# Optimization experiments

Hardware: AMD Instinct MI355X
Metric: run time of the kernel (lower is better)

The kernel has to match this reference:

```python
import jax, jax.numpy as jnp
import numpy as np

T, B, S = 8, 4, 2048
LAT, SYM, NC = 1024, 256, 512


def setup_inputs() -> dict:
    key = jax.random.key(0)
    ks = jax.random.split(key, 16)
    inp = {
        "token_state": jax.random.normal(ks[0], (B, S, LAT), jnp.float32),
        "bus_symbols": jax.random.normal(ks[1], (T, B, S, SYM), jnp.float32),
        "bus_indices": jax.random.randint(ks[2], (T, B, S), 0, NC),
        "bus_outputs": jax.random.normal(ks[3], (T, B, S, LAT), jnp.float32),
        "bus_mask": jnp.zeros((T,), jnp.bool_),
        # parameters (stored as (in, out) matrices)
        "Wq": jax.random.normal(ks[4], (SYM, 1), jnp.float32) / np.sqrt(SYM),
        "bq": jnp.zeros((1,), jnp.float32),
        "Wread": jax.random.normal(ks[5], (2 * LAT, LAT), jnp.float32) / np.sqrt(2 * LAT),
        "bread": jnp.zeros((LAT,), jnp.float32),
        "Wsym": jax.random.normal(ks[6], (LAT, SYM), jnp.float32) / np.sqrt(LAT),
        "bsym": jnp.zeros((SYM,), jnp.float32),
        "Wc1": jax.random.normal(ks[7], (LAT + SYM, LAT), jnp.float32) / np.sqrt(LAT + SYM),
        "bc1": jnp.zeros((LAT,), jnp.float32),
        "Wc2": jax.random.normal(ks[8], (LAT, LAT), jnp.float32) / np.sqrt(LAT),
        "bc2": jnp.zeros((LAT,), jnp.float32),
        "codebook": jax.random.normal(ks[9], (NC, SYM), jnp.float32),
    }
    return inp


def reference(token_state, bus_symbols, bus_indices, bus_outputs, bus_mask,
              Wq, bq, Wread, bread, Wsym, bsym, Wc1, bc1, Wc2, bc2, codebook):
    Tm, Bb, Ss, Dsym = bus_symbols.shape
    N = Bb * Ss
    syms = bus_symbols.reshape(Tm, N, Dsym)          # [T, N, SYM]
    outs = bus_outputs.reshape(Tm, N, -1)            # [T, N, LAT]

    # top-1 bus message routing
    relevance = (syms @ Wq + bq)[..., 0]             # [T, N]
    top_msg_idx = jnp.argmax(relevance, axis=0)      # [N]
    chosen = jnp.take_along_axis(outs, top_msg_idx[None, :, None], axis=0)[0]  # [N, LAT]
    bus_context = chosen.reshape(Bb, Ss, -1)

    z = jnp.concatenate([token_state, bus_context], axis=-1)
    z_read = z @ Wread + bread                       # [B, S, LAT]
    raw_symbol = z_read @ Wsym + bsym                # [B, S, SYM]

    # VQ: cdist argmin (squared distance has same argmin)
    flat = raw_symbol.reshape(-1, Dsym)              # [N, SYM]
    d2 = (jnp.sum(flat * flat, axis=1, keepdims=True)
          - 2.0 * flat @ codebook.T
          + jnp.sum(codebook * codebook, axis=1)[None, :])  # [N, NC]
    indices = jnp.argmin(d2, axis=-1)                # [N]
    quantized = codebook[indices].reshape(Bb, Ss, Dsym)

    h = jax.nn.relu(jnp.concatenate([z_read, quantized], axis=-1) @ Wc1 + bc1)
    node_output = h @ Wc2 + bc2 + token_state

    used_counts = jnp.zeros((Tm,), jnp.int32).at[top_msg_idx].add(1)
    keep_mask = used_counts == 0
    return node_output, quantized, indices.reshape(Bb, Ss), keep_mask
```

## Files before the change

kernel.cpp:

```cpp
#include <hip/hip_runtime.h>
#include <hip/hip_bf16.h>

#define DEVI __device__ __forceinline__

namespace {

constexpr int T_   = 8;
constexpr int NTOK = 8192;
constexpr int LAT  = 1024;
constexpr int SYM  = 256;
constexpr int NC   = 512;
constexpr float TAU = 0.6f;

typedef short short8 __attribute__((ext_vector_type(8)));
typedef float floatx4 __attribute__((ext_vector_type(4)));

DEVI unsigned short f2bf(float f){
  union { float f; unsigned u; } v; v.f = f;
  return (unsigned short)((v.u + 0x7fffu + ((v.u >> 16) & 1u)) >> 16);
}

DEVI void gload_lds16(const void* g, void* l){
  __builtin_amdgcn_global_load_lds((const __attribute__((address_space(1))) void*)g,
                                   (__attribute__((address_space(3))) void*)l, 16, 0, 0);
}

__global__ void route_k(const float* __restrict__ syms, const float* __restrict__ Wq,
                        int* __restrict__ top, int* __restrict__ counts){
  int gt = blockIdx.x * blockDim.x + threadIdx.x;
  int wid = gt >> 6, lane = gt & 63;
  if (wid >= NTOK) return;
  float4 wq = *(const float4*)(Wq + lane * 4);
  float best = -INFINITY; int bt = 0;
  for (int t = 0; t < T_; ++t){
    float4 s = *(const float4*)(syms + ((size_t)t * NTOK + wid) * SYM + lane * 4);
    float p = s.x*wq.x + s.y*wq.y + s.z*wq.z + s.w*wq.w;
    #pragma unroll
    for (int off = 32; off; off >>= 1) p += __shfl_down(p, off, 64);
    p = __shfl(p, 0, 64);
    if (p > best){ best = p; bt = t; }
  }
  if (lane == 0){ top[wid] = bt; atomicAdd(&counts[bt], 1); }
}

__global__ void cbt_k(const float* __restrict__ cb, float* __restrict__ cbT,
                      const int* __restrict__ counts, float* __restrict__ out_mask){
  int i = blockIdx.x * blockDim.x + threadIdx.x;
  if (i < NC * SYM){ int c = i / SYM, k = i % SYM; cbT[k * NC + c] = cb[i]; }
  if (blockIdx.x == 0 && threadIdx.x < T_)
    out_mask[threadIdx.x] = (counts[threadIdx.x] == 0) ? 1.0f : 0.0f;
}

__global__ void cnorm_k(const float* __restrict__ cb, const float* __restrict__ bsym,
                        float* __restrict__ cnorm, float* __restrict__ svec,
                        const float* __restrict__ bread, const float* __restrict__ Wsym,
                        float* __restrict__ rb){
  if (blockIdx.x == NC/4){
    int t = threadIdx.x;
    float a0=0.f,a1=0.f,a2=0.f,a3=0.f;
    for (int k = 0; k < LAT; k += 4){
      a0 += bread[k+0] * Wsym[(size_t)(k+0) * SYM + t];
      a1 += bread[k+1] * Wsym[(size_t)(k+1) * SYM + t];
      a2 += bread[k+2] * Wsym[(size_t)(k+2) * SYM + t];
      a3 += bread[k+3] * Wsym[(size_t)(k+3) * SYM + t];
    }
    rb[t] = bsym[t] + ((a0+a1)+(a2+a3));
    return;
  }
  int gt = blockIdx.x * blockDim.x + threadIdx.x;
  int wid = gt >> 6, lane = gt & 63;
  if (wid >= NC) return;
  float4 v = *(const float4*)(cb + (size_t)wid * SYM + lane * 4);
  float4 b = *(const float4*)(bsym + lane * 4);
  float p = v.x*v.x + v.y*v.y + v.z*v.z + v.w*v.w;
  float q = v.x*(v.x-2.f*b.x) + v.y*(v.y-2.f*b.y) + v.z*(v.z-2.f*b.z) + v.w*(v.w-2.f*b.w);
  #pragma unroll
  for (int off = 32; off; off >>= 1){ p += __shfl_down(p, off, 64); q += __shfl_down(q, off, 64); }
  if (lane == 0){ cnorm[wid] = p; svec[wid] = q; }
}

__global__ void t32multi_k(const float* __restrict__ Wread, unsigned short* __restrict__ WreadT,
                           const float* __restrict__ Wc1,   unsigned short* __restrict__ Wc1T,
                           const float* __restrict__ Wc2,   unsigned short* __restrict__ Wc2T){
  __shared__ float tile[32][33];
  int b = blockIdx.x;
  const float* in; unsigned short* out; int R, C, t;
  if (b < 2048){ in = Wread; out = WreadT; R = 2*LAT; C = LAT; t = b; }
  else if (b < 2048+1280){ in = Wc1; out = Wc1T; R = LAT+SYM; C = LAT; t = b - 2048; }
  else { in = Wc2; out = Wc2T; R = LAT; C = LAT; t = b - 3328; }
  int bx = t % 32, by = t / 32;
  int r0 = by * 32, c0 = bx * 32;
  int tid = threadIdx.x;
  int tx = tid & 31, ty = tid >> 5;
  #pragma unroll
  for (int j = 0; j < 4; ++j)
    tile[ty + j*8][tx] = in[(size_t)(r0 + ty + j*8) * C + c0 + tx];
  __syncthreads();
  #pragma unroll
  for (int j = 0; j < 4; ++j)
    out[(size_t)(c0 + ty + j*8) * R + r0 + tx] = f2bf(tile[tx][ty + j*8]);
}

template<int BM, int BN, int BK, int TM, int TN, int TB>
__global__ __launch_bounds__((BM/TM)*(BN/TN))
void gemm_f32(const float* __restrict__ A, const float* __restrict__ Bm,
              float* __restrict__ Cf, unsigned short* __restrict__ Ct,
              int M, int N, int K)
{
  constexpr int NT  = (BM/TM)*(BN/TN);
  constexpr int BMp = BM + 4, BNp = BN + 4;
  constexpr int KV  = BK / 4;
  constexpr int NLA = BM * KV;
  constexpr int NLB = (BK * BN) / 4;
  __shared__ float As[BK][BMp];
  __shared__ float Bs[BK][BNp];
  const int tid = threadIdx.x;
  const int tx = tid % (BN / TN), ty = tid / (BN / TN);
  const int m0 = blockIdx.x * BM, n0 = blockIdx.y * BN;
  float acc[TM][TN] = {};
  for (int k0 = 0; k0 < K; k0 += BK){
    for (int q = tid; q < NLA; q += NT){
      int m = q / KV, kq = (q % KV) * 4;
      float4 v = *(const float4*)(A + (size_t)(m0+m) * K + k0 + kq);
      As[kq+0][m] = v.x; As[kq+1][m] = v.y; As[kq+2][m] = v.z; As[kq+3][m] = v.w;
    }
    for (int q = tid; q < NLB; q += NT){
      int k = q / (BN/4), n4 = (q % (BN/4)) * 4;
      *(float4*)&Bs[k][n4] = *(const float4*)(Bm + (size_t)(k0+k) * N + n0 + n4);
    }
    __syncthreads();
    #pragma unroll
    for (int k = 0; k < BK; ++k){
      float a[TM], b[TN];
      #pragma unroll
      for (int i = 0; i < TM; ++i) a[i] = As[k][ty*TM + i];
      #pragma unroll
      for (int j = 0; j < TN; ++j) b[j] = Bs[k][tx*TN + j];
      #pragma unroll
      for (int i = 0; i < TM; ++i)
        #pragma unroll
        for (int j = 0; j < TN; ++j) acc[i][j] += a[i] * b[j];
    }
    __syncthreads();
  }
  #pragma unroll
  for (int i = 0; i < TM; ++i)
    #pragma unroll
    for (int j = 0; j < TN; ++j){
      if constexpr (TB){
        Ct[(size_t)(n0 + tx*TN + j) * M + m0 + ty*TM + i] = f2bf(acc[i][j]);
      } else {
        Cf[(size_t)(m0 + ty*TM + i) * N + n0 + tx*TN + j] = acc[i][j];
      }
    }
}

constexpr int A_PLAIN = 0, A_CAT = 1, A_F32CAT = 2;
constexpr int EP_ZH = 0, EP_VQ = 1, EP_RELU = 2, EP_OUT = 3;

template<int ASRC, int EPI>
__global__ __launch_bounds__(256)
void mgemm(const unsigned short* __restrict__ A, const unsigned short* __restrict__ A2,
           const unsigned short* __restrict__ BT, const float* __restrict__ bias,
           const float* __restrict__ resid,
           unsigned short* __restrict__ Cb, float* __restrict__ Cf,
           int N, int K, int asplit,
           const float* __restrict__ Af, const float* __restrict__ A2f,
           const int* __restrict__ topp)
{
  __shared__ unsigned short As[128*32];
  __shared__ unsigned short Bs[128*32];
  __shared__ int topl[128];
  const int tid  = threadIdx.x;
  const int wave = tid >> 6, lane = tid & 63;
  const int wy = wave >> 1, wx = wave & 1;
  const int lq = lane >> 4, lr = lane & 15;
  const int m0 = blockIdx.y * 128, n0 = blockIdx.x * 128;

  if constexpr (ASRC == A_F32CAT){
    if (tid < 128) topl[tid] = topp[m0 + tid];
    __syncthreads();
  }

  floatx4 acc[4][4] = {};

  for (int k0 = 0; k0 < K; k0 += 32){
    #pragma unroll
    for (int c = 0; c < 2; ++c){
      int chunk = tid + c*256;
      int mrel = chunk >> 2, kc = (chunk & 3) * 8;
      int gk = k0 + kc;
      if constexpr (ASRC == A_F32CAT){
        const float* sf;
        if (gk < asplit) sf = Af + (size_t)(m0+mrel) * asplit + gk;
        else sf = A2f + ((size_t)topl[mrel] * NTOK + (m0+mrel)) * (size_t)(K-asplit) + (gk-asplit);
        float4 v0 = *(const float4*)sf;
        float4 v1 = *(const float4*)(sf + 4);
        short8 o;
        o[0]=(short)f2bf(v0.x); o[1]=(short)f2bf(v0.y); o[2]=(short)f2bf(v0.z); o[3]=(short)f2bf(v0.w);
        o[4]=(short)f2bf(v1.x); o[5]=(short)f2bf(v1.y); o[6]=(short)f2bf(v1.z); o[7]=(short)f2bf(v1.w);
        *(short8*)&As[chunk*8] = o;
      } else {
        const unsigned short* srcA;
        if constexpr (ASRC == A_CAT){
          if (gk < asplit) srcA = A  + (size_t)(m0+mrel) * asplit + gk;
          else             srcA = A2 + (size_t)(m0+mrel) * (K-asplit) + (gk-asplit);
        } else {
          srcA = A + (size_t)(m0+mrel) * K + gk;
        }
        gload_lds16(srcA, &As[(c*256 + wave*64) * 8]);
      }
      gload_lds16(BT + (size_t)(n0+mrel) * K + gk, &Bs[(c*256 + wave*64) * 8]);
    }
    __syncthreads();
    short8 af[4], bf[4];
    #pragma unroll
    for (int i = 0; i < 4; ++i){
      af[i] = *(const short8*)&As[(wy*64 + i*16 + lr)*32 + lq*8];
      bf[i] = *(const short8*)&Bs[(wx*64 + i*16 + lr)*32 + lq*8];
    }
    #pragma unroll
    for (int i = 0; i < 4; ++i)
      #pragma unroll
      for (int j = 0; j < 4; ++j)
        acc[i][j] = __builtin_amdgcn_mfma_f32_16x16x32_bf16(af[i], bf[j], acc[i][j], 0, 0, 0);
    __syncthreads();
  }

  #pragma unroll
  for (int i = 0; i < 4; ++i){
    #pragma unroll
    for (int j = 0; j < 4; ++j){
      int gn = n0 + wx*64 + j*16 + lr;
      #pragma unroll
      for (int r = 0; r < 4; ++r){
        int gm = m0 + wy*64 + i*16 + lq*4 + r;
        float v = acc[i][j][r];
        if constexpr (EPI == EP_ZH){
          Cb[(size_t)gm * N + gn] = f2bf(v + bias[gn]);
        } else if constexpr (EPI == EP_VQ){
          Cf[(size_t)gm * N + gn] = bias[gn] - 2.f * v;
        } else if constexpr (EPI == EP_RELU){
          float u = v + bias[gn];
          Cb[(size_t)gm * N + gn] = f2bf(u > 0.f ? u : 0.f);
        } else {
          Cf[(size_t)gm * N + gn] = v + bias[gn] + resid[(size_t)gm * N + gn];
        }
      }
    }
  }
}

__global__ void vq_k(const float* __restrict__ scores, const float* __restrict__ cb,
                     float* __restrict__ out_q, float* __restrict__ out_idx,
                     unsigned short* __restrict__ q_h,
                     int* __restrict__ rcount, int* __restrict__ rlist){
  int gt = blockIdx.x * blockDim.x + threadIdx.x;
  int wid = gt >> 6, lane = gt & 63;
  if (wid >= NTOK) return;
  const float* row = scores + (size_t)wid * NC;
  float v1 = INFINITY, v2 = INFINITY; int i1 = 0x7fffffff;
  #pragma unroll
  for (int i = 0; i < NC/64; ++i){
    int c = i*64 + lane;
    float v = row[c];
    if (v < v1){ v2 = v1; v1 = v; i1 = c; } else v2 = fminf(v2, v);
  }
  #pragma unroll
  for (int off = 32; off; off >>= 1){
    float ov1 = __shfl_down(v1, off, 64);
    int   oi1 = __shfl_down(i1, off, 64);
    float ov2 = __shfl_down(v2, off, 64);
    float rest;
    if (ov1 < v1 || (ov1 == v1 && oi1 < i1)){ rest = v1; v1 = ov1; i1 = oi1; }
    else rest = ov1;
    v2 = fminf(fminf(v2, ov2), rest);
  }
  i1 = __shfl(i1, 0, 64);
  if (lane == 0){
    out_idx[wid] = (float)i1;
    if (__shfl(v2, 0, 64) - __shfl(v1, 0, 64) < TAU){
      int p = atomicAdd(rcount, 1); rlist[p] = wid;
    }
  }
  float4 cv = *(const float4*)(cb + (size_t)i1 * SYM + lane * 4);
  *(float4*)(out_q + (size_t)wid * SYM + lane * 4) = cv;
  ushort4 qh; qh.x = f2bf(cv.x); qh.y = f2bf(cv.y); qh.z = f2bf(cv.z); qh.w = f2bf(cv.w);
  *(ushort4*)(q_h + (size_t)wid * SYM + lane * 4) = qh;
}

constexpr int RT = 4;

__global__ __launch_bounds__(256)
void repair_k(const int* __restrict__ rcount, const int* __restrict__ rlist,
              const int* __restrict__ top,
              const float* __restrict__ ts, const float* __restrict__ bus,
              const float* __restrict__ Wcomb, const float* __restrict__ rb,
              const float* __restrict__ cb, const float* __restrict__ cnorm,
              float* __restrict__ out_q, float* __restrict__ out_idx,
              unsigned short* __restrict__ q_h){
  __shared__ float a[RT][2*LAT];
  __shared__ float raw[RT][SYM];
  __shared__ float pv[RT][4];
  __shared__ int   pi[RT][4];
  __shared__ int   fidx[RT];
  int tid = threadIdx.x;
  int lane = tid & 63, wave = tid >> 6;
  int cnt = *rcount;
  int nchunk = (cnt + RT - 1) / RT;
  for (int ch = blockIdx.x; ch < nchunk; ch += gridDim.x){
    int base = ch * RT;
    int nt = min(RT, cnt - base);
    for (int q = tid; q < nt * 512; q += 256){
      int t = q >> 9, c = (q & 511) * 4;
      int m = rlist[base + t];
      int tp = top[m];
      float4 v = (c < LAT) ? *(const float4*)(ts + (size_t)m * LAT + c)
                           : *(const float4*)(bus + ((size_t)tp * NTOK + m) * LAT + (c - LAT));
      *(float4*)&a[t][c] = v;
    }
    __syncthreads();
    float acc0[RT], acc1[RT], acc2[RT], acc3[RT];
    #pragma unroll
    for (int t = 0; t < RT; ++t){ acc0[t]=0.f; acc1[t]=0.f; acc2[t]=0.f; acc3[t]=0.f; }
    for (int k = 0; k < 2*LAT; k += 4){
      float w0 = Wcomb[(size_t)(k+0) * SYM + tid];
      float w1 = Wcomb[(size_t)(k+1) * SYM + tid];
      float w2 = Wcomb[(size_t)(k+2) * SYM + tid];
      float w3 = Wcomb[(size_t)(k+3) * SYM + tid];
      #pragma unroll
      for (int t = 0; t < RT; ++t){
        float4 av = *(const float4*)&a[t][k];
        acc0[t] += av.x * w0; acc1[t] += av.y * w1;
        acc2[t] += av.z * w2; acc3[t] += av.w * w3;
      }
    }
    #pragma unroll
    for (int t = 0; t < RT; ++t)
      raw[t][tid] = rb[tid] + ((acc0[t] + acc1[t]) + (acc2[t] + acc3[t]));
    __syncthreads();
    float bv[RT]; int bi[RT];
    #pragma unroll
    for (int t = 0; t < RT; ++t){ bv[t] = INFINITY; bi[t] = 0x7fffffff; }
    #pragma unroll
    for (int cc = 0; cc < 2; ++cc){
      int c = tid + cc * 256;
      const float* cr = cb + (size_t)c * SYM;
      float d[RT] = {};
      for (int j = 0; j < SYM; j += 4){
        float4 cv = *(const float4*)(cr + j);
        #pragma unroll
        for (int t = 0; t < RT; ++t){
          float4 rv4 = *(const float4*)&raw[t][j];
          d[t] += rv4.x*cv.x + rv4.y*cv.y + rv4.z*cv.z + rv4.w*cv.w;
        }
      }
      #pragma unroll
      for (int t = 0; t < RT; ++t){
        float s = cnorm[c] - 2.f * d[t];
        if (s < bv[t] || (s == bv[t] && c < bi[t])){ bv[t] = s; bi[t] = c; }
      }
    }
    #pragma unroll
    for (int t = 0; t < RT; ++t){
      float v = bv[t]; int i = bi[t];
      #pragma unroll
      for (int off = 32; off; off >>= 1){
        float ov = __shfl_down(v, off, 64);
        int   oi = __shfl_down(i, off, 64);
        if (ov < v || (ov == v && oi < i)){ v = ov; i = oi; }
      }
      if (lane == 0){ pv[t][wave] = v; pi[t][wave] = i; }
    }
    __syncthreads();
    if (tid < nt){
      float v = pv[tid][0]; int i = pi[tid][0];
      #pragma unroll
      for (int w = 1; w < 4; ++w){
        if (pv[tid][w] < v || (pv[tid][w] == v && pi[tid][w] < i)){ v = pv[tid][w]; i = pi[tid][w]; }
      }
      fidx[tid] = i;
      out_idx[rlist[base + tid]] = (float)i;
    }
    __syncthreads();
    for (int t = 0; t < nt; ++t){
      int m = rlist[base + t];
      int idx = fidx[t];
      float cvv = cb[(size_t)idx * SYM + tid];
      out_q[(size_t)m * SYM + tid] = cvv;
      q_h[(size_t)m * SYM + tid] = f2bf(cvv);
    }
    __syncthreads();
  }
}

}

extern "C" void kernel_launch(void* const* d_in, const int* in_sizes, int n_in,
                              void* d_out, int out_size, void* d_ws, size_t ws_size,
                              hipStream_t stream){
  const float* token_state = (const float*)d_in[0];
  const float* bus_symbols = (const float*)d_in[1];
  const float* bus_outputs = (const float*)d_in[3];
  const float* Wq    = (const float*)d_in[5];
  const float* Wread = (const float*)d_in[7];
  const float* bread = (const float*)d_in[8];
  const float* Wsym  = (const float*)d_in[9];
  const float* bsym  = (const float*)d_in[10];
  const float* Wc1   = (const float*)d_in[11];
  const float* bc1   = (const float*)d_in[12];
  const float* Wc2   = (const float*)d_in[13];
  const float* bc2   = (const float*)d_in[14];
  const float* codebook = (const float*)d_in[15];

  float* out_node = (float*)d_out;
  float* out_quant= out_node + (size_t)NTOK * LAT;
  float* out_idx  = out_quant + (size_t)NTOK * SYM;
  float* out_mask = out_idx + NTOK;

  char* W = (char*)d_ws; size_t off = 0;
  auto alloc = [&](size_t bytes)->char*{ char* p = W + off; off = (off + bytes + 255) & ~(size_t)255; return p; };
  int*   top     = (int*)alloc(NTOK*4);
  char*  zeroed  = alloc(256);
  int*   counts  = (int*)zeroed;
  int*   rcount  = (int*)(zeroed + 128);
  int*   rlist   = (int*)alloc(NTOK*4);
  float* cbT     = (float*)alloc((size_t)SYM*NC*4);
  float* cnorm   = (float*)alloc(NC*4);
  float* svec    = (float*)alloc(NC*4);
  float* rb      = (float*)alloc(SYM*4);
  float* Wcomb   = (float*)alloc((size_t)2*LAT*SYM*4);
  unsigned short* WreadT = (unsigned short*)alloc((size_t)LAT*2*LAT*2);
  unsigned short* Wc1T   = (unsigned short*)alloc((size_t)LAT*(LAT+SYM)*2);
  unsigned short* Wc2T   = (unsigned short*)alloc((size_t)LAT*LAT*2);
  unsigned short* WfuseT = (unsigned short*)alloc((size_t)NC*LAT*2);
  unsigned short* z_h    = (unsigned short*)alloc((size_t)NTOK*LAT*2);
  unsigned short* q_h    = (unsigned short*)alloc((size_t)NTOK*SYM*2);
  unsigned short* h_h    = (unsigned short*)alloc((size_t)NTOK*LAT*2);
  float* scores          = (float*)alloc((size_t)NTOK*NC*4);

  hipMemsetAsync(zeroed, 0, 256, stream);

  route_k<<<NTOK/4, 256, 0, stream>>>(bus_symbols, Wq, top, counts);
  cbt_k<<<(NC*SYM)/256, 256, 0, stream>>>(codebook, cbT, counts, out_mask);
  cnorm_k<<<NC/4 + 1, 256, 0, stream>>>(codebook, bsym, cnorm, svec, bread, Wsym, rb);

  gemm_f32<64,64,8,4,4,1><<<dim3(LAT/64, NC/64), 256, 0, stream>>>(
      Wsym, cbT, nullptr, WfuseT, LAT, NC, SYM);
  gemm_f32<32,64,8,2,4,0><<<dim3(2*LAT/32, SYM/64), 256, 0, stream>>>(
      Wread, Wsym, Wcomb, nullptr, 2*LAT, SYM, LAT);
  t32multi_k<<<2048+1280+1024, 256, 0, stream>>>(Wread, WreadT, Wc1, Wc1T, Wc2, Wc2T);

  mgemm<A_F32CAT, EP_ZH><<<dim3(LAT/128, NTOK/128), 256, 0, stream>>>(
      nullptr, nullptr, WreadT, bread, nullptr, z_h, nullptr, LAT, 2*LAT, LAT,
      token_state, bus_outputs, top);
  mgemm<A_PLAIN, EP_VQ><<<dim3(NC/128, NTOK/128), 256, 0, stream>>>(
      z_h, nullptr, WfuseT, svec, nullptr, nullptr, scores, NC, LAT, 0,
      nullptr, nullptr, nullptr);

  vq_k<<<NTOK/4, 256, 0, stream>>>(scores, codebook, out_quant, out_idx, q_h, rcount, rlist);
  repair_k<<<512, 256, 0, stream>>>(rcount, rlist, top, token_state, bus_outputs,
                                    Wcomb, rb, codebook, cnorm, out_quant, out_idx, q_h);

  mgemm<A_CAT, EP_RELU><<<dim3(LAT/128, NTOK/128), 256, 0, stream>>>(
      z_h, q_h, Wc1T, bc1, nullptr, h_h, nullptr, LAT, LAT+SYM, LAT,
      nullptr, nullptr, nullptr);
  mgemm<A_PLAIN, EP_OUT><<<dim3(LAT/128, NTOK/128), 256, 0, stream>>>(
      h_h, nullptr, Wc2T, bc2, token_state, nullptr, out_node, LAT, LAT, 0,
      nullptr, nullptr, nullptr);
}
```

Measured before the change: 966.5 us.

## Pre-pack gathered bf16 A operand and swizzle GEMM workgroup order

```diff
diff --git a/kernel.cpp b/kernel.cpp
--- a/kernel.cpp
+++ b/kernel.cpp
@@ -99,6 +99,17 @@
   #pragma unroll
   for (int j = 0; j < 4; ++j)
     out[(size_t)(c0 + ty + j*8) * R + r0 + tx] = f2bf(tile[tx][ty + j*8]);
+}
+
+__global__ void pack_az(const float* __restrict__ ts, const float* __restrict__ bus,
+                        const int* __restrict__ top, unsigned short* __restrict__ Az){
+  int id = blockIdx.x * blockDim.x + threadIdx.x;
+  int m = id >> 9, c = (id & 511) * 4;
+  const float* src = (c < LAT) ? (ts + (size_t)m * LAT + c)
+                               : (bus + ((size_t)top[m] * NTOK + m) * LAT + (c - LAT));
+  float4 v = *(const float4*)src;
+  ushort4 o; o.x = f2bf(v.x); o.y = f2bf(v.y); o.z = f2bf(v.z); o.w = f2bf(v.w);
+  *(ushort4*)(Az + (size_t)m * (2*LAT) + c) = o;
 }
 
 template<int BM, int BN, int BK, int TM, int TN, int TB>
@@ -155,7 +166,7 @@
     }
 }
 
-constexpr int A_PLAIN = 0, A_CAT = 1, A_F32CAT = 2;
+constexpr int A_PLAIN = 0, A_CAT = 1;
 constexpr int EP_ZH = 0, EP_VQ = 1, EP_RELU = 2, EP_OUT = 3;
 
 template<int ASRC, int EPI>
@@ -164,23 +175,20 @@
            const unsigned short* __restrict__ BT, const float* __restrict__ bias,
            const float* __restrict__ resid,
            unsigned short* __restrict__ Cb, float* __restrict__ Cf,
-           int N, int K, int asplit,
-           const float* __restrict__ Af, const float* __restrict__ A2f,
-           const int* __restrict__ topp)
+           int N, int K, int asplit)
 {
   __shared__ unsigned short As[128*32];
   __shared__ unsigned short Bs[128*32];
-  __shared__ int topl[128];
   const int tid  = threadIdx.x;
   const int wave = tid >> 6, lane = tid & 63;
   const int wy = wave >> 1, wx = wave & 1;
   const int lq = lane >> 4, lr = lane & 15;
-  const int m0 = blockIdx.y * 128, n0 = blockIdx.x * 128;
-
-  if constexpr (ASRC == A_F32CAT){
-    if (tid < 128) topl[tid] = topp[m0 + tid];
-    __syncthreads();
-  }
+
+  const int nwg  = gridDim.x * gridDim.y;
+  const int orig = blockIdx.y * gridDim.x + blockIdx.x;
+  const int dec  = (orig & 7) * (nwg >> 3) + (orig >> 3);
+  const int bx   = dec % gridDim.x, by = dec / gridDim.x;
+  const int m0 = by * 128, n0 = bx * 128;
 
   floatx4 acc[4][4] = {};
 
@@ -190,26 +198,14 @@
       int chunk = tid + c*256;
       int mrel = chunk >> 2, kc = (chunk & 3) * 8;
       int gk = k0 + kc;
-      if constexpr (ASRC == A_F32CAT){
-        const float* sf;
-        if (gk < asplit) sf = Af + (size_t)(m0+mrel) * asplit + gk;
-        else sf = A2f + ((size_t)topl[mrel] * NTOK + (m0+mrel)) * (size_t)(K-asplit) + (gk-asplit);
-        float4 v0 = *(const float4*)sf;
-        float4 v1 = *(const float4*)(sf + 4);
-        short8 o;
-        o[0]=(short)f2bf(v0.x); o[1]=(short)f2bf(v0.y); o[2]=(short)f2bf(v0.z); o[3]=(short)f2bf(v0.w);
-        o[4]=(short)f2bf(v1.x); o[5]=(short)f2bf(v1.y); o[6]=(short)f2bf(v1.z); o[7]=(short)f2bf(v1.w);
-        *(short8*)&As[chunk*8] = o;
+      const unsigned short* srcA;
+      if constexpr (ASRC == A_CAT){
+        if (gk < asplit) srcA = A  + (size_t)(m0+mrel) * asplit + gk;
+        else             srcA = A2 + (size_t)(m0+mrel) * (K-asplit) + (gk-asplit);
       } else {
-        const unsigned short* srcA;
-        if constexpr (ASRC == A_CAT){
-          if (gk < asplit) srcA = A  + (size_t)(m0+mrel) * asplit + gk;
-          else             srcA = A2 + (size_t)(m0+mrel) * (K-asplit) + (gk-asplit);
-        } else {
-          srcA = A + (size_t)(m0+mrel) * K + gk;
-        }
-        gload_lds16(srcA, &As[(c*256 + wave*64) * 8]);
-      }
+        srcA = A + (size_t)(m0+mrel) * K + gk;
+      }
+      gload_lds16(srcA, &As[(c*256 + wave*64) * 8]);
       gload_lds16(BT + (size_t)(n0+mrel) * K + gk, &Bs[(c*256 + wave*64) * 8]);
     }
     __syncthreads();
@@ -437,7 +433,9 @@
   unsigned short* z_h    = (unsigned short*)alloc((size_t)NTOK*LAT*2);
   unsigned short* q_h    = (unsigned short*)alloc((size_t)NTOK*SYM*2);
   unsigned short* h_h    = (unsigned short*)alloc((size_t)NTOK*LAT*2);
-  float* scores          = (float*)alloc((size_t)NTOK*NC*4);
+  char* az_region        = alloc((size_t)NTOK*2*LAT*2);
+  unsigned short* A_z    = (unsigned short*)az_region;
+  float* scores          = (float*)az_region;
 
   hipMemsetAsync(zeroed, 0, 256, stream);
 
@@ -451,21 +449,19 @@
       Wread, Wsym, Wcomb, nullptr, 2*LAT, SYM, LAT);
   t32multi_k<<<2048+1280+1024, 256, 0, stream>>>(Wread, WreadT, Wc1, Wc1T, Wc2, Wc2T);
 
-  mgemm<A_F32CAT, EP_ZH><<<dim3(LAT/128, NTOK/128), 256, 0, stream>>>(
-      nullptr, nullptr, WreadT, bread, nullptr, z_h, nullptr, LAT, 2*LAT, LAT,
-      token_state, bus_outputs, top);
+  pack_az<<<(NTOK*512)/256, 256, 0, stream>>>(token_state, bus_outputs, top, A_z);
+
+  mgemm<A_PLAIN, EP_ZH><<<dim3(LAT/128, NTOK/128), 256, 0, stream>>>(
+      A_z, nullptr, WreadT, bread, nullptr, z_h, nullptr, LAT, 2*LAT, 0);
   mgemm<A_PLAIN, EP_VQ><<<dim3(NC/128, NTOK/128), 256, 0, stream>>>(
-      z_h, nullptr, WfuseT, svec, nullptr, nullptr, scores, NC, LAT, 0,
-      nullptr, nullptr, nullptr);
+      z_h, nullptr, WfuseT, svec, nullptr, nullptr, scores, NC, LAT, 0);
 
   vq_k<<<NTOK/4, 256, 0, stream>>>(scores, codebook, out_quant, out_idx, q_h, rcount, rlist);
   repair_k<<<512, 256, 0, stream>>>(rcount, rlist, top, token_state, bus_outputs,
                                     Wcomb, rb, codebook, cnorm, out_quant, out_idx, q_h);
 
   mgemm<A_CAT, EP_RELU><<<dim3(LAT/128, NTOK/128), 256, 0, stream>>>(
-      z_h, q_h, Wc1T, bc1, nullptr, h_h, nullptr, LAT, LAT+SYM, LAT,
-      nullptr, nullptr, nullptr);
+      z_h, q_h, Wc1T, bc1, nullptr, h_h, nullptr, LAT, LAT+SYM, LAT);
   mgemm<A_PLAIN, EP_OUT><<<dim3(LAT/128, NTOK/128), 256, 0, stream>>>(
-      h_h, nullptr, Wc2T, bc2, token_state, nullptr, out_node, LAT, LAT, 0,
-      nullptr, nullptr, nullptr);
-}
+      h_h, nullptr, Wc2T, bc2, token_state, nullptr, out_node, LAT, LAT, 0);
+}
```

After: 905.9 us. -6.3%, faster.
